# Kernel optimization log

Measured on AMD Instinct MI355X. Metric: run time of the kernel, lower is better.

## Reference

```python
import jax, jax.numpy as jnp
import numpy as np

COLB = 16            # COL_BLOCK_WIDTH
IN_W = 1024          # input_width; zero_inputs=0 so input_locations = arange(IN_W)
OUT_W = 512          # output_width
DEPTH = 8            # network_depth
IN_L = 4             # butterfly_in_depth
OUT_L = 4            # butterfly_out_depth
ACT = 8              # activations_per_block
BLOCKS = 64          # blocks_per_layer -> num_inputs = 1024 per module
CURV = 1.0
GROW = BLOCKS * ACT  # 512 new rows per module
TOTAL = IN_W + DEPTH * GROW  # 5120
BATCH = 4096


def setup_inputs() -> dict:
    key = jax.random.key(0)
    k1, k2, k3 = jax.random.split(key, 3)
    input_data = jax.random.normal(k1, (IN_W, BATCH), dtype=jnp.float32)
    scales = jnp.full((IN_W,), 0.05, dtype=jnp.float32)
    # angles uniform in (-pi, pi), shape [depth, in_layers+out_layers, num_inputs/2]
    angles = (jax.random.uniform(k2, (DEPTH, IN_L + OUT_L, BLOCKS * COLB // 2)) * 2.0 - 1.0) * np.pi
    angles = angles.astype(jnp.float32)
    biases = jax.random.normal(k3, (DEPTH, GROW), dtype=jnp.float32) * 0.05
    # per-module indices_in = randperm(total_width_so_far)[:num_inputs]
    rng = np.random.RandomState(0)
    tw = IN_W
    idxs = []
    for _ in range(DEPTH):
        idxs.append(rng.permutation(tw)[: BLOCKS * COLB].astype(np.int32))
        tw += GROW
    indices_in = jnp.asarray(np.stack(idxs))  # [depth, 1024]
    return {"input_data": input_data, "scales": scales, "angles": angles,
            "biases": biases, "indices_in": indices_in}


def _rotate(x, ang, stride):
    # x: [W, B]; pair row i (with (i//stride)%2==0) with row i+stride inside 16-blocks
    W, B = x.shape
    xr = x.reshape(W // (2 * stride), 2, stride, B)
    a = ang.reshape(W // (2 * stride), stride)[:, :, None]
    c, s = jnp.cos(a), jnp.sin(a)
    lo, hi = xr[:, 0], xr[:, 1]              # [W/2s, s, B]
    nlo = c * lo + s * hi
    nhi = -s * lo + c * hi
    return jnp.stack([nlo, nhi], axis=1).reshape(W, B)


def _butterfly_module(data, ang, bias, idx, idx_out):
    W = BLOCKS * COLB
    x = data[idx]                             # gather [1024, B]
    for l in range(IN_L):
        x = _rotate(x, ang[l], 2 ** (l % 4))
    xb = x.reshape(BLOCKS, COLB, -1)
    pre = xb[:, :ACT, :] + bias.reshape(BLOCKS, ACT)[:, :, None]
    # curvature (smoothed-ReLU) activation
    act = 0.5 * (pre + jnp.sqrt(pre * pre + CURV * CURV))
    xb = xb.at[:, :ACT, :].set(act)
    x = xb.reshape(W, -1)
    for l in range(OUT_L):
        x = _rotate(x, ang[IN_L + l], 2 ** ((IN_L + l) % 4))
    data = data.at[idx].set(x)                # scatter working set back
    data = data.at[idx_out: idx_out + GROW].set(act.reshape(GROW, -1))
    return data


def reference(input_data, scales, angles, biases, indices_in):
    B = input_data.shape[1]
    data = jnp.zeros((TOTAL, B), dtype=input_data.dtype)
    data = data.at[:IN_W].set(scales[:, None] * input_data)
    for i in range(DEPTH):
        data = _butterfly_module(data, angles[i], biases[i], indices_in[i], IN_W + GROW * i)
    return data[TOTAL - OUT_W:]
```

## Files before the change

kernel.cpp:

```cpp
#include <hip/hip_runtime.h>
#include <math.h>

#define N_INW     1024
#define N_DEPTH   8
#define N_GROW    512
#define N_BATCH   4096
#define N_THREADS 128
#define N_LAYERS  64
#define SLAB_B    19584

typedef __attribute__((ext_vector_type(2))) float    F2;
typedef __attribute__((ext_vector_type(2))) _Float16 h2;

__global__ void precompute_kernel(const float* __restrict__ angles,
                                  const int*   __restrict__ indices,
                                  _Float16* __restrict__ csh,
                                  int*   __restrict__ addrs) {
    int i = blockIdx.x * blockDim.x + threadIdx.x;
    if (i < N_LAYERS * 512) {
        int g = i >> 9, p = i & 511, blk = p >> 3, j = p & 7;
        float a = angles[i];
        _Float16* base = csh + g * 1024 + blk * 16;
        base[j]     = (_Float16)cosf(a);
        base[8 + j] = (_Float16)sinf(a);
    }
    if (i < N_DEPTH * N_INW) {
        int v = indices[i];
        addrs[i] = (v + (v >> 4)) << 2;
    }
}

#define ADDR(r) ((((r) + ((r) >> 4))) << 2)

#define LDH(A)    __builtin_bit_cast(h2, *(const unsigned*)(L + (A)))
#define STH(A, V) do { *(unsigned*)(L + (A)) =                                 \
                       __builtin_bit_cast(unsigned, (V)); } while (0)

#define PKU(x, y) __builtin_bit_cast(unsigned int,                             \
                      __builtin_amdgcn_cvt_pkrtz((x), (y)))

#define BCL(U) ({ h2 _t = __builtin_bit_cast(h2, (unsigned)(U));               \
                  h2 _r; _r.x = _t.x; _r.y = _t.x; _r; })
#define BCH(U) ({ h2 _t = __builtin_bit_cast(h2, (unsigned)(U));               \
                  h2 _r; _r.x = _t.y; _r.y = _t.y; _r; })

#define ROTPH(LO, HI, CC, SS) do { h2 _l = LO, _h = HI, _c = CC, _s = SS;      \
    LO = _c * _l + _s * _h; HI = _c * _h - _s * _l; } while (0)

#define DECL_SET(P)                                                            \
    uint4 P##c0, P##s0, P##c1, P##s1, P##c2, P##s2, P##c3, P##s3,              \
          P##c4, P##s4, P##c5, P##s5, P##c6, P##s6, P##c7, P##s7;              \
    int4  P##i0, P##i1, P##i2, P##i3;                                          \
    float4 P##bA, P##bB;

#define SYN1(P, K, ANB) do {                                                   \
    const float4* _p = (const float4*)((ANB) + (K)*512 + (blk << 3));          \
    float4 _u = _p[0], _v = _p[1];                                             \
    float _c0,_c1,_c2,_c3,_c4,_c5,_c6,_c7,_t0,_t1,_t2,_t3,_t4,_t5,_t6,_t7;     \
    __sincosf(_u.x,&_t0,&_c0); __sincosf(_u.y,&_t1,&_c1);                      \
    __sincosf(_u.z,&_t2,&_c2); __sincosf(_u.w,&_t3,&_c3);                      \
    __sincosf(_v.x,&_t4,&_c4); __sincosf(_v.y,&_t5,&_c5);                      \
    __sincosf(_v.z,&_t6,&_c6); __sincosf(_v.w,&_t7,&_c7);                      \
    P##c##K = make_uint4(PKU(_c0,_c1),PKU(_c2,_c3),PKU(_c4,_c5),PKU(_c6,_c7)); \
    P##s##K = make_uint4(PKU(_t0,_t1),PKU(_t2,_t3),PKU(_t4,_t5),PKU(_t6,_t7)); \
  } while (0)

#define LOADCS1(P, K, CSN, ANB) do { if (USE_TABLE) {                          \
    const char* _b = (CSN) + (blk << 5) + (K)*2048;                            \
    P##c##K = *(const uint4*)(_b); P##s##K = *(const uint4*)(_b + 16);         \
  } else { SYN1(P, K, ANB); } } while (0)

#define LOADCS8(P, CSN, ANB) do {                                              \
    LOADCS1(P,0,CSN,ANB); LOADCS1(P,1,CSN,ANB); LOADCS1(P,2,CSN,ANB);          \
    LOADCS1(P,3,CSN,ANB); LOADCS1(P,4,CSN,ANB); LOADCS1(P,5,CSN,ANB);          \
    LOADCS1(P,6,CSN,ANB); LOADCS1(P,7,CSN,ANB); } while (0)
#define LOADCS4(P, CSN, ANB) do {                                              \
    LOADCS1(P,0,CSN,ANB); LOADCS1(P,1,CSN,ANB); LOADCS1(P,2,CSN,ANB);          \
    LOADCS1(P,3,CSN,ANB); } while (0)

#define TR(v) (((v) + ((v) >> 4)) << 2)
#define LOAD_AB(P, ATN, INB, BIN) do { if (USE_TABLE) {                        \
    const int4* _ip = (const int4*)((ATN) + (blk << 4));                       \
    P##i0=_ip[0]; P##i1=_ip[1]; P##i2=_ip[2]; P##i3=_ip[3];                    \
  } else {                                                                     \
    const int4* _ip = (const int4*)((INB) + (blk << 4));                       \
    int4 _v0=_ip[0], _v1=_ip[1], _v2=_ip[2], _v3=_ip[3];                       \
    P##i0.x=TR(_v0.x); P##i0.y=TR(_v0.y); P##i0.z=TR(_v0.z); P##i0.w=TR(_v0.w);\
    P##i1.x=TR(_v1.x); P##i1.y=TR(_v1.y); P##i1.z=TR(_v1.z); P##i1.w=TR(_v1.w);\
    P##i2.x=TR(_v2.x); P##i2.y=TR(_v2.y); P##i2.z=TR(_v2.z); P##i2.w=TR(_v2.w);\
    P##i3.x=TR(_v3.x); P##i3.y=TR(_v3.y); P##i3.z=TR(_v3.z); P##i3.w=TR(_v3.w);\
  }                                                                            \
  const float4* _bp = (const float4*)((BIN) + (blk << 3));                     \
  P##bA = _bp[0]; P##bB = _bp[1]; } while (0)

#define HROTS1(C,S) do {                                                       \
    ROTPH(x0,x1,  BCL(C.x),BCL(S.x)); ROTPH(x2,x3,  BCH(C.x),BCH(S.x));        \
    ROTPH(x4,x5,  BCL(C.y),BCL(S.y)); ROTPH(x6,x7,  BCH(C.y),BCH(S.y));        \
    ROTPH(x8,x9,  BCL(C.z),BCL(S.z)); ROTPH(x10,x11,BCH(C.z),BCH(S.z));        \
    ROTPH(x12,x13,BCL(C.w),BCL(S.w)); ROTPH(x14,x15,BCH(C.w),BCH(S.w));        \
  } while (0)
#define HROTS2(C,S) do {                                                       \
    ROTPH(x0,x2,  BCL(C.x),BCL(S.x)); ROTPH(x1,x3,  BCH(C.x),BCH(S.x));        \
    ROTPH(x4,x6,  BCL(C.y),BCL(S.y)); ROTPH(x5,x7,  BCH(C.y),BCH(S.y));        \
    ROTPH(x8,x10, BCL(C.z),BCL(S.z)); ROTPH(x9,x11, BCH(C.z),BCH(S.z));        \
    ROTPH(x12,x14,BCL(C.w),BCL(S.w)); ROTPH(x13,x15,BCH(C.w),BCH(S.w));        \
  } while (0)
#define HROTS4(C,S) do {                                                       \
    ROTPH(x0,x4,  BCL(C.x),BCL(S.x)); ROTPH(x1,x5,  BCH(C.x),BCH(S.x));        \
    ROTPH(x2,x6,  BCL(C.y),BCL(S.y)); ROTPH(x3,x7,  BCH(C.y),BCH(S.y));        \
    ROTPH(x8,x12, BCL(C.z),BCL(S.z)); ROTPH(x9,x13, BCH(C.z),BCH(S.z));        \
    ROTPH(x10,x14,BCL(C.w),BCL(S.w)); ROTPH(x11,x15,BCH(C.w),BCH(S.w));        \
  } while (0)
#define HROTS8(C,S) do {                                                       \
    ROTPH(x0,x8,  BCL(C.x),BCL(S.x)); ROTPH(x1,x9,  BCH(C.x),BCH(S.x));        \
    ROTPH(x2,x10, BCL(C.y),BCL(S.y)); ROTPH(x3,x11, BCH(C.y),BCH(S.y));        \
    ROTPH(x4,x12, BCL(C.z),BCL(S.z)); ROTPH(x5,x13, BCH(C.z),BCH(S.z));        \
    ROTPH(x6,x14, BCL(C.w),BCL(S.w)); ROTPH(x7,x15, BCH(C.w),BCH(S.w));        \
  } while (0)

#define HROT(P, K, M) M(P##c##K, P##s##K)

#define ACTH(X, BF) do {                                                       \
    float _lo = (float)(X).x + (BF), _hi = (float)(X).y + (BF);                \
    _lo = 0.5f * (_lo + __builtin_amdgcn_sqrtf(_lo * _lo + 1.0f));             \
    _hi = 0.5f * (_hi + __builtin_amdgcn_sqrtf(_hi * _hi + 1.0f));             \
    X = __builtin_bit_cast(h2, PKU(_lo, _hi)); } while (0)

#define FENCE() __builtin_amdgcn_sched_barrier(0)

#define PROC_MOD(P, N, CSN, ANN, ATN, INB, BIN, M, FULL) do {                  \
  const int a0=P##i0.x, a1=P##i0.y, a2=P##i0.z, a3=P##i0.w,                    \
            a4=P##i1.x, a5=P##i1.y, a6=P##i1.z, a7=P##i1.w,                    \
            a8=P##i2.x, a9=P##i2.y, a10=P##i2.z, a11=P##i2.w,                  \
            a12=P##i3.x, a13=P##i3.y, a14=P##i3.z, a15=P##i3.w;                \
  h2 x0=LDH(a0), x1=LDH(a1), x2=LDH(a2), x3=LDH(a3),                           \
     x4=LDH(a4), x5=LDH(a5), x6=LDH(a6), x7=LDH(a7),                           \
     x8=LDH(a8), x9=LDH(a9), x10=LDH(a10), x11=LDH(a11),                       \
     x12=LDH(a12), x13=LDH(a13), x14=LDH(a14), x15=LDH(a15);                   \
  if (FULL) { LOADCS8(N, CSN, ANN); } else { LOADCS4(N, CSN, ANN); }           \
  FENCE();                                                                     \
  HROT(P,0,HROTS1); HROT(P,1,HROTS2); HROT(P,2,HROTS4); HROT(P,3,HROTS8);      \
  ACTH(x0,P##bA.x); ACTH(x1,P##bA.y); ACTH(x2,P##bA.z); ACTH(x3,P##bA.w);      \
  ACTH(x4,P##bB.x); ACTH(x5,P##bB.y); ACTH(x6,P##bB.z); ACTH(x7,P##bB.w);      \
  const int _ab = ADDR(N_INW + (M)*N_GROW + (blk << 3));                       \
  STH(_ab+ 0,x0); STH(_ab+ 4,x1); STH(_ab+ 8,x2); STH(_ab+12,x3);              \
  STH(_ab+16,x4); STH(_ab+20,x5); STH(_ab+24,x6); STH(_ab+28,x7);              \
  LOAD_AB(N, ATN, INB, BIN);                                                   \
  FENCE();                                                                     \
  HROT(P,4,HROTS1); HROT(P,5,HROTS2); HROT(P,6,HROTS4); HROT(P,7,HROTS8);      \
  STH(a0,x0);  STH(a1,x1);  STH(a2,x2);  STH(a3,x3);                           \
  STH(a4,x4);  STH(a5,x5);  STH(a6,x6);  STH(a7,x7);                           \
  STH(a8,x8);  STH(a9,x9);  STH(a10,x10); STH(a11,x11);                        \
  STH(a12,x12); STH(a13,x13); STH(a14,x14); STH(a15,x15);                      \
} while (0)

template <bool USE_TABLE>
__global__ __launch_bounds__(N_THREADS, 2)
void butterfly_fused_kernel(const float* __restrict__ input,
                            const float* __restrict__ scales,
                            const float* __restrict__ biases,
                            const int*   __restrict__ indices,
                            const char*  __restrict__ cs_tab,
                            const int*   __restrict__ addr_tab,
                            const float* __restrict__ angles,
                            float* __restrict__ out) {
    extern __shared__ float ldsbuf[];
    const int t   = threadIdx.x;
    const int blk = t & 63;
    const int cp  = t >> 6;
    char* L = (char*)ldsbuf + cp * SLAB_B;
    const int b   = blockIdx.x;
    const int cg  = ((((b & 7) * 128) + (b >> 3)) << 2) + (cp << 1);

    DECL_SET(A) DECL_SET(B)

    LOADCS8(A, cs_tab, angles);
    LOAD_AB(A, addr_tab, indices, biases);

#pragma unroll
    for (int k = 0; k < 16; ++k) {
        const int r = (k << 6) + blk;
        F2 v = *(const F2*)(input + (size_t)r * N_BATCH + cg);
        STH(ADDR(r), __builtin_bit_cast(h2, PKU(scales[r] * v.x, scales[r] * v.y)));
    }

    const char*  csn = cs_tab + 16384;
    const float* ann = angles + 4096;
    const int*   atn = addr_tab + N_INW;
    const int*   inb = indices + N_INW;
    const float* bin = biases + N_GROW;

#pragma unroll 1
    for (int tt = 0; tt < 3; ++tt) {
        const int m = 2 * tt;
        PROC_MOD(A, B, csn, ann, atn, inb, bin, m, 1);
        csn += 16384; ann += 4096; atn += N_INW; inb += N_INW; bin += N_GROW;
        PROC_MOD(B, A, csn, ann, atn, inb, bin, m + 1, 1);
        csn += 16384; ann += 4096; atn += N_INW; inb += N_INW; bin += N_GROW;
    }
    PROC_MOD(A, B, csn, ann, atn, inb, bin, 6, 0);

    {
        h2 x0=LDH(Bi0.x), x1=LDH(Bi0.y), x2=LDH(Bi0.z), x3=LDH(Bi0.w),
           x4=LDH(Bi1.x), x5=LDH(Bi1.y), x6=LDH(Bi1.z), x7=LDH(Bi1.w),
           x8=LDH(Bi2.x), x9=LDH(Bi2.y), x10=LDH(Bi2.z), x11=LDH(Bi2.w),
           x12=LDH(Bi3.x), x13=LDH(Bi3.y), x14=LDH(Bi3.z), x15=LDH(Bi3.w);
        FENCE();
        HROT(B,0,HROTS1); HROT(B,1,HROTS2); HROT(B,2,HROTS4); HROT(B,3,HROTS8);
        ACTH(x0,BbA.x); ACTH(x1,BbA.y); ACTH(x2,BbA.z); ACTH(x3,BbA.w);
        ACTH(x4,BbB.x); ACTH(x5,BbB.y); ACTH(x6,BbB.z); ACTH(x7,BbB.w);
#define OUTW(J, X) do { F2 _o; _o.x = (float)(X).x; _o.y = (float)(X).y;       \
        *(F2*)(out + (size_t)((blk<<3)+(J))*N_BATCH + cg) = _o; } while (0)
        OUTW(0,x0); OUTW(1,x1); OUTW(2,x2); OUTW(3,x3);
        OUTW(4,x4); OUTW(5,x5); OUTW(6,x6); OUTW(7,x7);
#undef OUTW
    }
}

extern "C" void kernel_launch(void* const* d_in, const int* in_sizes, int n_in,
                              void* d_out, int out_size, void* d_ws, size_t ws_size,
                              hipStream_t stream) {
    const float* input   = (const float*)d_in[0];
    const float* scales  = (const float*)d_in[1];
    const float* angles  = (const float*)d_in[2];
    const float* biases  = (const float*)d_in[3];
    const int*   indices = (const int*)d_in[4];
    float* out = (float*)d_out;

    const size_t cs_bytes  = (size_t)N_LAYERS * 2048;
    const size_t adr_bytes = (size_t)N_DEPTH * N_INW * sizeof(int);
    const size_t lds_bytes = (size_t)2 * SLAB_B;
    const int grid = N_BATCH / 4;

    if (ws_size >= cs_bytes + adr_bytes) {
        _Float16* csh = (_Float16*)d_ws;
        int* addrs = (int*)((char*)d_ws + cs_bytes);
        precompute_kernel<<<(N_LAYERS * 512 + 255) / 256, 256, 0, stream>>>(
            angles, indices, csh, addrs);
        butterfly_fused_kernel<true><<<grid, N_THREADS, lds_bytes, stream>>>(
            input, scales, biases, indices, (const char*)csh, addrs, angles, out);
    } else {
        butterfly_fused_kernel<false><<<grid, N_THREADS, lds_bytes, stream>>>(
            input, scales, biases, indices, nullptr, nullptr, angles, out);
    }
}
```

Before: 97.56 us.

## Switch to one batch column per wave with row-packed fp16 LDS layout

Each wave now owns a single batch column instead of two. The LDS slab is halved and 256-thread blocks are used, with four waves per block. Pairs of adjacent rows are packed into half2 registers, so the stride-1 rotation runs as an intra-register op_sel packed FMA in inline asm and the other strides use packed math. Gather and scatter now use 16-bit LDS accesses, and the address table is compressed to 16-bit packed pairs. The aim is to halve register pressure and raise occupancy, at the cost of twice as many narrow LDS accesses and uncoalesced scalar global loads and stores.

```diff
diff --git a/kernel.cpp b/kernel.cpp
--- a/kernel.cpp
+++ b/kernel.cpp
@@ -5,17 +5,19 @@
 #define N_DEPTH   8
 #define N_GROW    512
 #define N_BATCH   4096
-#define N_THREADS 128
+#define N_THREADS 256
 #define N_LAYERS  64
-#define SLAB_B    19584
+#define SLAB_B    9792
 
 typedef __attribute__((ext_vector_type(2))) float    F2;
 typedef __attribute__((ext_vector_type(2))) _Float16 h2;
+
+#define ADDR(r) (((r) << 1) + (((r) >> 5) << 2))
 
 __global__ void precompute_kernel(const float* __restrict__ angles,
                                   const int*   __restrict__ indices,
                                   _Float16* __restrict__ csh,
-                                  int*   __restrict__ addrs) {
+                                  unsigned short* __restrict__ addrs) {
     int i = blockIdx.x * blockDim.x + threadIdx.x;
     if (i < N_LAYERS * 512) {
         int g = i >> 9, p = i & 511, blk = p >> 3, j = p & 7;
@@ -26,194 +28,176 @@
     }
     if (i < N_DEPTH * N_INW) {
         int v = indices[i];
-        addrs[i] = (v + (v >> 4)) << 2;
+        addrs[i] = (unsigned short)ADDR(v);
     }
 }
-
-#define ADDR(r) ((((r) + ((r) >> 4))) << 2)
-
-#define LDH(A)    __builtin_bit_cast(h2, *(const unsigned*)(L + (A)))
-#define STH(A, V) do { *(unsigned*)(L + (A)) =                                 \
-                       __builtin_bit_cast(unsigned, (V)); } while (0)
 
 #define PKU(x, y) __builtin_bit_cast(unsigned int,                             \
                       __builtin_amdgcn_cvt_pkrtz((x), (y)))
 
-#define BCL(U) ({ h2 _t = __builtin_bit_cast(h2, (unsigned)(U));               \
-                  h2 _r; _r.x = _t.x; _r.y = _t.x; _r; })
-#define BCH(U) ({ h2 _t = __builtin_bit_cast(h2, (unsigned)(U));               \
-                  h2 _r; _r.x = _t.y; _r.y = _t.y; _r; })
-
-#define ROTPH(LO, HI, CC, SS) do { h2 _l = LO, _h = HI, _c = CC, _s = SS;      \
+#define FENCE() __builtin_amdgcn_sched_barrier(0)
+
+
+#define ROT1_L(X, CW, SW) do { unsigned _t;                                    \
+    asm("v_pk_mul_f16 %1, %3, %0 op_sel:[0,1] op_sel_hi:[0,0]\n\t"             \
+        "v_pk_fma_f16 %0, %2, %0, %1 op_sel:[0,0,0] op_sel_hi:[0,1,1] "        \
+            "neg_hi:[0,0,1]"                                                   \
+        : "+v"(X), "=&v"(_t) : "v"(CW), "v"(SW)); } while (0)
+#define ROT1_H(X, CW, SW) do { unsigned _t;                                    \
+    asm("v_pk_mul_f16 %1, %3, %0 op_sel:[1,1] op_sel_hi:[1,0]\n\t"             \
+        "v_pk_fma_f16 %0, %2, %0, %1 op_sel:[1,0,0] op_sel_hi:[1,1,1] "        \
+            "neg_hi:[0,0,1]"                                                   \
+        : "+v"(X), "=&v"(_t) : "v"(CW), "v"(SW)); } while (0)
+
+#define ROTPH(LO, HI, CW, SW) do {                                             \
+    h2 _c = __builtin_bit_cast(h2, (unsigned)(CW));                            \
+    h2 _s = __builtin_bit_cast(h2, (unsigned)(SW));                            \
+    h2 _l = LO, _h = HI;                                                       \
     LO = _c * _l + _s * _h; HI = _c * _h - _s * _l; } while (0)
 
-#define DECL_SET(P)                                                            \
-    uint4 P##c0, P##s0, P##c1, P##s1, P##c2, P##s2, P##c3, P##s3,              \
-          P##c4, P##s4, P##c5, P##s5, P##c6, P##s6, P##c7, P##s7;              \
-    int4  P##i0, P##i1, P##i2, P##i3;                                          \
-    float4 P##bA, P##bB;
-
-#define SYN1(P, K, ANB) do {                                                   \
-    const float4* _p = (const float4*)((ANB) + (K)*512 + (blk << 3));          \
+#define ROT4(C0,S0,C1,S1,C2,S2,C3,S3) do {                                     \
+    ROT1_L(x0,C0.x,S0.x); ROT1_H(x1,C0.x,S0.x);                                \
+    ROT1_L(x2,C0.y,S0.y); ROT1_H(x3,C0.y,S0.y);                                \
+    ROT1_L(x4,C0.z,S0.z); ROT1_H(x5,C0.z,S0.z);                                \
+    ROT1_L(x6,C0.w,S0.w); ROT1_H(x7,C0.w,S0.w);                                \
+    ROTPH(x0,x1,C1.x,S1.x); ROTPH(x2,x3,C1.y,S1.y);                            \
+    ROTPH(x4,x5,C1.z,S1.z); ROTPH(x6,x7,C1.w,S1.w);                            \
+    ROTPH(x0,x2,C2.x,S2.x); ROTPH(x1,x3,C2.y,S2.y);                            \
+    ROTPH(x4,x6,C2.z,S2.z); ROTPH(x5,x7,C2.w,S2.w);                            \
+    ROTPH(x0,x4,C3.x,S3.x); ROTPH(x1,x5,C3.y,S3.y);                            \
+    ROTPH(x2,x6,C3.z,S3.z); ROTPH(x3,x7,C3.w,S3.w);                            \
+  } while (0)
+
+#define LCS1(CV, SV, LIDX) do { if (USE_TABLE) {                               \
+    const char* _b = cs_tab + (size_t)(LIDX) * 2048 + (lane << 5);             \
+    CV = *(const uint4*)_b; SV = *(const uint4*)(_b + 16);                     \
+  } else {                                                                     \
+    const float4* _p = (const float4*)(angles + (size_t)(LIDX)*512 + (lane<<3));\
     float4 _u = _p[0], _v = _p[1];                                             \
     float _c0,_c1,_c2,_c3,_c4,_c5,_c6,_c7,_t0,_t1,_t2,_t3,_t4,_t5,_t6,_t7;     \
     __sincosf(_u.x,&_t0,&_c0); __sincosf(_u.y,&_t1,&_c1);                      \
     __sincosf(_u.z,&_t2,&_c2); __sincosf(_u.w,&_t3,&_c3);                      \
     __sincosf(_v.x,&_t4,&_c4); __sincosf(_v.y,&_t5,&_c5);                      \
     __sincosf(_v.z,&_t6,&_c6); __sincosf(_v.w,&_t7,&_c7);                      \
-    P##c##K = make_uint4(PKU(_c0,_c1),PKU(_c2,_c3),PKU(_c4,_c5),PKU(_c6,_c7)); \
-    P##s##K = make_uint4(PKU(_t0,_t1),PKU(_t2,_t3),PKU(_t4,_t5),PKU(_t6,_t7)); \
-  } while (0)
-
-#define LOADCS1(P, K, CSN, ANB) do { if (USE_TABLE) {                          \
-    const char* _b = (CSN) + (blk << 5) + (K)*2048;                            \
-    P##c##K = *(const uint4*)(_b); P##s##K = *(const uint4*)(_b + 16);         \
-  } else { SYN1(P, K, ANB); } } while (0)
-
-#define LOADCS8(P, CSN, ANB) do {                                              \
-    LOADCS1(P,0,CSN,ANB); LOADCS1(P,1,CSN,ANB); LOADCS1(P,2,CSN,ANB);          \
-    LOADCS1(P,3,CSN,ANB); LOADCS1(P,4,CSN,ANB); LOADCS1(P,5,CSN,ANB);          \
-    LOADCS1(P,6,CSN,ANB); LOADCS1(P,7,CSN,ANB); } while (0)
-#define LOADCS4(P, CSN, ANB) do {                                              \
-    LOADCS1(P,0,CSN,ANB); LOADCS1(P,1,CSN,ANB); LOADCS1(P,2,CSN,ANB);          \
-    LOADCS1(P,3,CSN,ANB); } while (0)
-
-#define TR(v) (((v) + ((v) >> 4)) << 2)
-#define LOAD_AB(P, ATN, INB, BIN) do { if (USE_TABLE) {                        \
-    const int4* _ip = (const int4*)((ATN) + (blk << 4));                       \
-    P##i0=_ip[0]; P##i1=_ip[1]; P##i2=_ip[2]; P##i3=_ip[3];                    \
+    CV = make_uint4(PKU(_c0,_c1),PKU(_c2,_c3),PKU(_c4,_c5),PKU(_c6,_c7));      \
+    SV = make_uint4(PKU(_t0,_t1),PKU(_t2,_t3),PKU(_t4,_t5),PKU(_t6,_t7));      \
+  } } while (0)
+
+#define LOAD_IN(M)  do { LCS1(cA0,sA0,(M)*8+0); LCS1(cA1,sA1,(M)*8+1);         \
+                         LCS1(cA2,sA2,(M)*8+2); LCS1(cA3,sA3,(M)*8+3); } while (0)
+#define LOAD_OUT(M) do { LCS1(cB0,sB0,(M)*8+4); LCS1(cB1,sB1,(M)*8+5);         \
+                         LCS1(cB2,sB2,(M)*8+6); LCS1(cB3,sB3,(M)*8+7); } while (0)
+
+#define A16(v)      (((v) << 1) + (((v) >> 5) << 2))
+#define PK2(lo, hi) (int)((unsigned)A16(lo) | ((unsigned)A16(hi) << 16))
+#define LOAD_ADDR(D0, D1, M) do { if (USE_TABLE) {                             \
+    const int4* _ap = (const int4*)(addr_tab + (size_t)(M)*2048 + (lane << 5));\
+    D0 = _ap[0]; D1 = _ap[1];                                                  \
   } else {                                                                     \
-    const int4* _ip = (const int4*)((INB) + (blk << 4));                       \
+    const int4* _ip = (const int4*)(indices + (size_t)(M)*N_INW + (lane << 4));\
     int4 _v0=_ip[0], _v1=_ip[1], _v2=_ip[2], _v3=_ip[3];                       \
-    P##i0.x=TR(_v0.x); P##i0.y=TR(_v0.y); P##i0.z=TR(_v0.z); P##i0.w=TR(_v0.w);\
-    P##i1.x=TR(_v1.x); P##i1.y=TR(_v1.y); P##i1.z=TR(_v1.z); P##i1.w=TR(_v1.w);\
-    P##i2.x=TR(_v2.x); P##i2.y=TR(_v2.y); P##i2.z=TR(_v2.z); P##i2.w=TR(_v2.w);\
-    P##i3.x=TR(_v3.x); P##i3.y=TR(_v3.y); P##i3.z=TR(_v3.z); P##i3.w=TR(_v3.w);\
-  }                                                                            \
-  const float4* _bp = (const float4*)((BIN) + (blk << 3));                     \
-  P##bA = _bp[0]; P##bB = _bp[1]; } while (0)
-
-#define HROTS1(C,S) do {                                                       \
-    ROTPH(x0,x1,  BCL(C.x),BCL(S.x)); ROTPH(x2,x3,  BCH(C.x),BCH(S.x));        \
-    ROTPH(x4,x5,  BCL(C.y),BCL(S.y)); ROTPH(x6,x7,  BCH(C.y),BCH(S.y));        \
-    ROTPH(x8,x9,  BCL(C.z),BCL(S.z)); ROTPH(x10,x11,BCH(C.z),BCH(S.z));        \
-    ROTPH(x12,x13,BCL(C.w),BCL(S.w)); ROTPH(x14,x15,BCH(C.w),BCH(S.w));        \
-  } while (0)
-#define HROTS2(C,S) do {                                                       \
-    ROTPH(x0,x2,  BCL(C.x),BCL(S.x)); ROTPH(x1,x3,  BCH(C.x),BCH(S.x));        \
-    ROTPH(x4,x6,  BCL(C.y),BCL(S.y)); ROTPH(x5,x7,  BCH(C.y),BCH(S.y));        \
-    ROTPH(x8,x10, BCL(C.z),BCL(S.z)); ROTPH(x9,x11, BCH(C.z),BCH(S.z));        \
-    ROTPH(x12,x14,BCL(C.w),BCL(S.w)); ROTPH(x13,x15,BCH(C.w),BCH(S.w));        \
-  } while (0)
-#define HROTS4(C,S) do {                                                       \
-    ROTPH(x0,x4,  BCL(C.x),BCL(S.x)); ROTPH(x1,x5,  BCH(C.x),BCH(S.x));        \
-    ROTPH(x2,x6,  BCL(C.y),BCL(S.y)); ROTPH(x3,x7,  BCH(C.y),BCH(S.y));        \
-    ROTPH(x8,x12, BCL(C.z),BCL(S.z)); ROTPH(x9,x13, BCH(C.z),BCH(S.z));        \
-    ROTPH(x10,x14,BCL(C.w),BCL(S.w)); ROTPH(x11,x15,BCH(C.w),BCH(S.w));        \
-  } while (0)
-#define HROTS8(C,S) do {                                                       \
-    ROTPH(x0,x8,  BCL(C.x),BCL(S.x)); ROTPH(x1,x9,  BCH(C.x),BCH(S.x));        \
-    ROTPH(x2,x10, BCL(C.y),BCL(S.y)); ROTPH(x3,x11, BCH(C.y),BCH(S.y));        \
-    ROTPH(x4,x12, BCL(C.z),BCL(S.z)); ROTPH(x5,x13, BCH(C.z),BCH(S.z));        \
-    ROTPH(x6,x14, BCL(C.w),BCL(S.w)); ROTPH(x7,x15, BCH(C.w),BCH(S.w));        \
-  } while (0)
-
-#define HROT(P, K, M) M(P##c##K, P##s##K)
-
-#define ACTH(X, BF) do {                                                       \
-    float _lo = (float)(X).x + (BF), _hi = (float)(X).y + (BF);                \
+    D0.x = PK2(_v0.x,_v0.y); D0.y = PK2(_v0.z,_v0.w);                          \
+    D0.z = PK2(_v1.x,_v1.y); D0.w = PK2(_v1.z,_v1.w);                          \
+    D1.x = PK2(_v2.x,_v2.y); D1.y = PK2(_v2.z,_v2.w);                          \
+    D1.z = PK2(_v3.x,_v3.y); D1.w = PK2(_v3.z,_v3.w);                          \
+  } } while (0)
+
+#define ALO(W) ((int)((unsigned)(W) & 0xffffu))
+#define AHI(W) ((int)((unsigned)(W) >> 16))
+
+#define GAT(R, W) do {                                                         \
+    unsigned _lo = *(const unsigned short*)(L + ALO(W));                       \
+    unsigned _hi = *(const unsigned short*)(L + AHI(W));                       \
+    x##R = __builtin_bit_cast(h2, _lo | (_hi << 16)); } while (0)
+
+#define SCAT(R, W) do {                                                        \
+    unsigned _u = __builtin_bit_cast(unsigned, x##R);                          \
+    *(unsigned short*)(L + ALO(W)) = (unsigned short)_u;                       \
+    *(unsigned short*)(L + AHI(W)) = (unsigned short)(_u >> 16); } while (0)
+
+#define ACTH(X, B0, B1) do {                                                   \
+    float _lo = (float)(X).x + (B0), _hi = (float)(X).y + (B1);                \
     _lo = 0.5f * (_lo + __builtin_amdgcn_sqrtf(_lo * _lo + 1.0f));             \
     _hi = 0.5f * (_hi + __builtin_amdgcn_sqrtf(_hi * _hi + 1.0f));             \
     X = __builtin_bit_cast(h2, PKU(_lo, _hi)); } while (0)
 
-#define FENCE() __builtin_amdgcn_sched_barrier(0)
-
-#define PROC_MOD(P, N, CSN, ANN, ATN, INB, BIN, M, FULL) do {                  \
-  const int a0=P##i0.x, a1=P##i0.y, a2=P##i0.z, a3=P##i0.w,                    \
-            a4=P##i1.x, a5=P##i1.y, a6=P##i1.z, a7=P##i1.w,                    \
-            a8=P##i2.x, a9=P##i2.y, a10=P##i2.z, a11=P##i2.w,                  \
-            a12=P##i3.x, a13=P##i3.y, a14=P##i3.z, a15=P##i3.w;                \
-  h2 x0=LDH(a0), x1=LDH(a1), x2=LDH(a2), x3=LDH(a3),                           \
-     x4=LDH(a4), x5=LDH(a5), x6=LDH(a6), x7=LDH(a7),                           \
-     x8=LDH(a8), x9=LDH(a9), x10=LDH(a10), x11=LDH(a11),                       \
-     x12=LDH(a12), x13=LDH(a13), x14=LDH(a14), x15=LDH(a15);                   \
-  if (FULL) { LOADCS8(N, CSN, ANN); } else { LOADCS4(N, CSN, ANN); }           \
-  FENCE();                                                                     \
-  HROT(P,0,HROTS1); HROT(P,1,HROTS2); HROT(P,2,HROTS4); HROT(P,3,HROTS8);      \
-  ACTH(x0,P##bA.x); ACTH(x1,P##bA.y); ACTH(x2,P##bA.z); ACTH(x3,P##bA.w);      \
-  ACTH(x4,P##bB.x); ACTH(x5,P##bB.y); ACTH(x6,P##bB.z); ACTH(x7,P##bB.w);      \
-  const int _ab = ADDR(N_INW + (M)*N_GROW + (blk << 3));                       \
-  STH(_ab+ 0,x0); STH(_ab+ 4,x1); STH(_ab+ 8,x2); STH(_ab+12,x3);              \
-  STH(_ab+16,x4); STH(_ab+20,x5); STH(_ab+24,x6); STH(_ab+28,x7);              \
-  LOAD_AB(N, ATN, INB, BIN);                                                   \
-  FENCE();                                                                     \
-  HROT(P,4,HROTS1); HROT(P,5,HROTS2); HROT(P,6,HROTS4); HROT(P,7,HROTS8);      \
-  STH(a0,x0);  STH(a1,x1);  STH(a2,x2);  STH(a3,x3);                           \
-  STH(a4,x4);  STH(a5,x5);  STH(a6,x6);  STH(a7,x7);                           \
-  STH(a8,x8);  STH(a9,x9);  STH(a10,x10); STH(a11,x11);                        \
-  STH(a12,x12); STH(a13,x13); STH(a14,x14); STH(a15,x15);                      \
-} while (0)
-
 template <bool USE_TABLE>
-__global__ __launch_bounds__(N_THREADS, 2)
+__global__ __launch_bounds__(N_THREADS, 4)
 void butterfly_fused_kernel(const float* __restrict__ input,
                             const float* __restrict__ scales,
                             const float* __restrict__ biases,
                             const int*   __restrict__ indices,
                             const char*  __restrict__ cs_tab,
-                            const int*   __restrict__ addr_tab,
+                            const char*  __restrict__ addr_tab,
                             const float* __restrict__ angles,
                             float* __restrict__ out) {
     extern __shared__ float ldsbuf[];
-    const int t   = threadIdx.x;
-    const int blk = t & 63;
-    const int cp  = t >> 6;
-    char* L = (char*)ldsbuf + cp * SLAB_B;
+    const int t    = threadIdx.x;
+    const int lane = t & 63;
+    const int w    = t >> 6;
+    char* L = (char*)ldsbuf + w * SLAB_B;
     const int b   = blockIdx.x;
-    const int cg  = ((((b & 7) * 128) + (b >> 3)) << 2) + (cp << 1);
-
-    DECL_SET(A) DECL_SET(B)
-
-    LOADCS8(A, cs_tab, angles);
-    LOAD_AB(A, addr_tab, indices, biases);
+    const int cg  = ((((b & 7) * 128) + (b >> 3)) << 2) + w;
+
+    uint4 cA0,sA0,cA1,sA1,cA2,sA2,cA3,sA3;
+    uint4 cB0,sB0,cB1,sB1,cB2,sB2,cB3,sB3;
+    int4  ad0, ad1;
+    h2 x0, x1, x2, x3, x4, x5, x6, x7;
+
+    LOAD_IN(0);
+    LOAD_ADDR(ad0, ad1, 0);
 
 #pragma unroll
-    for (int k = 0; k < 16; ++k) {
-        const int r = (k << 6) + blk;
-        F2 v = *(const F2*)(input + (size_t)r * N_BATCH + cg);
-        STH(ADDR(r), __builtin_bit_cast(h2, PKU(scales[r] * v.x, scales[r] * v.y)));
-    }
-
-    const char*  csn = cs_tab + 16384;
-    const float* ann = angles + 4096;
-    const int*   atn = addr_tab + N_INW;
-    const int*   inb = indices + N_INW;
-    const float* bin = biases + N_GROW;
+    for (int k = 0; k < 8; ++k) {
+        const int r = (k << 7) + (lane << 1);
+        F2 sc = *(const F2*)(scales + r);
+        float v0 = input[(size_t)r * N_BATCH + cg] * sc.x;
+        float v1 = input[(size_t)(r + 1) * N_BATCH + cg] * sc.y;
+        *(unsigned*)(L + ADDR(r)) = PKU(v0, v1);
+    }
 
 #pragma unroll 1
-    for (int tt = 0; tt < 3; ++tt) {
-        const int m = 2 * tt;
-        PROC_MOD(A, B, csn, ann, atn, inb, bin, m, 1);
-        csn += 16384; ann += 4096; atn += N_INW; inb += N_INW; bin += N_GROW;
-        PROC_MOD(B, A, csn, ann, atn, inb, bin, m + 1, 1);
-        csn += 16384; ann += 4096; atn += N_INW; inb += N_INW; bin += N_GROW;
-    }
-    PROC_MOD(A, B, csn, ann, atn, inb, bin, 6, 0);
+    for (int m = 0; m < 7; ++m) {
+        int4 nad0, nad1;
+        LOAD_OUT(m);
+        const float4* _bp = (const float4*)(biases + (size_t)m * N_GROW + (lane << 3));
+        float4 bb0 = _bp[0], bb1 = _bp[1];
+        GAT(0, ad0.x); GAT(1, ad0.y); GAT(2, ad0.z); GAT(3, ad0.w);
+        GAT(4, ad1.x); GAT(5, ad1.y); GAT(6, ad1.z); GAT(7, ad1.w);
+        FENCE();
+        ROT4(cA0,sA0,cA1,sA1,cA2,sA2,cA3,sA3);
+        ACTH(x0, bb0.x, bb0.y); ACTH(x1, bb0.z, bb0.w);
+        ACTH(x2, bb1.x, bb1.y); ACTH(x3, bb1.z, bb1.w);
+        {
+            const int _ab = ADDR(N_INW + m * N_GROW + (lane << 3));
+            *(unsigned*)(L + _ab + 0)  = __builtin_bit_cast(unsigned, x0);
+            *(unsigned*)(L + _ab + 4)  = __builtin_bit_cast(unsigned, x1);
+            *(unsigned*)(L + _ab + 8)  = __builtin_bit_cast(unsigned, x2);
+            *(unsigned*)(L + _ab + 12) = __builtin_bit_cast(unsigned, x3);
+        }
+        LOAD_IN(m + 1);
+        LOAD_ADDR(nad0, nad1, m + 1);
+        FENCE();
+        ROT4(cB0,sB0,cB1,sB1,cB2,sB2,cB3,sB3);
+        SCAT(0, ad0.x); SCAT(1, ad0.y); SCAT(2, ad0.z); SCAT(3, ad0.w);
+        SCAT(4, ad1.x); SCAT(5, ad1.y); SCAT(6, ad1.z); SCAT(7, ad1.w);
+        ad0 = nad0; ad1 = nad1;
+    }
 
     {
-        h2 x0=LDH(Bi0.x), x1=LDH(Bi0.y), x2=LDH(Bi0.z), x3=LDH(Bi0.w),
-           x4=LDH(Bi1.x), x5=LDH(Bi1.y), x6=LDH(Bi1.z), x7=LDH(Bi1.w),
-           x8=LDH(Bi2.x), x9=LDH(Bi2.y), x10=LDH(Bi2.z), x11=LDH(Bi2.w),
-           x12=LDH(Bi3.x), x13=LDH(Bi3.y), x14=LDH(Bi3.z), x15=LDH(Bi3.w);
+        const float4* _bp = (const float4*)(biases + (size_t)7 * N_GROW + (lane << 3));
+        float4 bb0 = _bp[0], bb1 = _bp[1];
+        GAT(0, ad0.x); GAT(1, ad0.y); GAT(2, ad0.z); GAT(3, ad0.w);
+        GAT(4, ad1.x); GAT(5, ad1.y); GAT(6, ad1.z); GAT(7, ad1.w);
         FENCE();
-        HROT(B,0,HROTS1); HROT(B,1,HROTS2); HROT(B,2,HROTS4); HROT(B,3,HROTS8);
-        ACTH(x0,BbA.x); ACTH(x1,BbA.y); ACTH(x2,BbA.z); ACTH(x3,BbA.w);
-        ACTH(x4,BbB.x); ACTH(x5,BbB.y); ACTH(x6,BbB.z); ACTH(x7,BbB.w);
-#define OUTW(J, X) do { F2 _o; _o.x = (float)(X).x; _o.y = (float)(X).y;       \
-        *(F2*)(out + (size_t)((blk<<3)+(J))*N_BATCH + cg) = _o; } while (0)
-        OUTW(0,x0); OUTW(1,x1); OUTW(2,x2); OUTW(3,x3);
-        OUTW(4,x4); OUTW(5,x5); OUTW(6,x6); OUTW(7,x7);
-#undef OUTW
+        ROT4(cA0,sA0,cA1,sA1,cA2,sA2,cA3,sA3);
+        ACTH(x0, bb0.x, bb0.y); ACTH(x1, bb0.z, bb0.w);
+        ACTH(x2, bb1.x, bb1.y); ACTH(x3, bb1.z, bb1.w);
+        float* op = out + (size_t)(lane << 3) * N_BATCH + cg;
+        op[0 * N_BATCH] = (float)x0.x; op[1 * N_BATCH] = (float)x0.y;
+        op[2 * N_BATCH] = (float)x1.x; op[3 * N_BATCH] = (float)x1.y;
+        op[4 * N_BATCH] = (float)x2.x; op[5 * N_BATCH] = (float)x2.y;
+        op[6 * N_BATCH] = (float)x3.x; op[7 * N_BATCH] = (float)x3.y;
     }
 }
 
@@ -228,17 +212,18 @@
     float* out = (float*)d_out;
 
     const size_t cs_bytes  = (size_t)N_LAYERS * 2048;
-    const size_t adr_bytes = (size_t)N_DEPTH * N_INW * sizeof(int);
-    const size_t lds_bytes = (size_t)2 * SLAB_B;
+    const size_t adr_bytes = (size_t)N_DEPTH * N_INW * 2;
+    const size_t lds_bytes = (size_t)4 * SLAB_B;
     const int grid = N_BATCH / 4;
 
     if (ws_size >= cs_bytes + adr_bytes) {
         _Float16* csh = (_Float16*)d_ws;
-        int* addrs = (int*)((char*)d_ws + cs_bytes);
+        unsigned short* addrs = (unsigned short*)((char*)d_ws + cs_bytes);
         precompute_kernel<<<(N_LAYERS * 512 + 255) / 256, 256, 0, stream>>>(
             angles, indices, csh, addrs);
         butterfly_fused_kernel<true><<<grid, N_THREADS, lds_bytes, stream>>>(
-            input, scales, biases, indices, (const char*)csh, addrs, angles, out);
+            input, scales, biases, indices, (const char*)csh, (const char*)addrs,
+            angles, out);
     } else {
         butterfly_fused_kernel<false><<<grid, N_THREADS, lds_bytes, stream>>>(
             input, scales, biases, indices, nullptr, nullptr, angles, out);
```

Measured after the change: 111.6 us. +14.4%, slower.
